# Performance work log

Measured on AMD Instinct MI355X. Metric: run time of the kernel, lower is better.

The kernel has to match this reference:

```python
import jax, jax.numpy as jnp
import numpy as np

N_STATES = 35
EMIT_SCALE = -500.0


def _constants():
    prior = jnp.full((N_STATES,), -10.0, dtype=jnp.float32).at[0].set(10.0)
    eye = jnp.eye(N_STATES, dtype=jnp.float32)
    trans = (0.1 * eye
             + 0.8 * jnp.roll(eye, 1, axis=1)
             + 0.08 * jnp.roll(eye, 2, axis=1)
             + (0.02 / N_STATES) * jnp.ones((N_STATES, N_STATES), dtype=jnp.float32))
    # Categorical(probs=trans).logits == log of row-normalized probs
    log_trans = jnp.log(trans / trans.sum(axis=-1, keepdims=True))
    return prior, log_trans


def setup_inputs() -> dict:
    key = jax.random.key(0)
    k1, k2 = jax.random.split(key)
    observations = jax.random.normal(k1, (64, 512, 16, 13, 12), dtype=jnp.float32)
    obs_matrix = jax.random.uniform(k2, (35, 16, 13, 12), dtype=jnp.float32)
    return {"observations": observations, "obs_matrix": obs_matrix}


def reference(observations, obs_matrix):
    prior, log_trans = _constants()
    B, T = observations.shape[:2]
    D = 16 * 13 * 12  # flattened frame dim = 2496
    x = observations.reshape(B, T, D)           # [B,T,D]
    m = obs_matrix.reshape(N_STATES, D)         # [S,D]
    x_sq = jnp.sum(x * x, axis=-1)              # [B,T]
    m_sq = jnp.sum(m * m, axis=-1)              # [S]
    xm = jnp.einsum('btd,sd->bts', x, m)        # [B,T,S]
    emis = (x_sq[..., None] + m_sq[None, None, :] - 2.0 * xm) / EMIT_SCALE  # [B,T,S]

    alpha0 = emis[:, 0] + prior                 # [B,S]
    log_trans_T = log_trans.T                   # [j,i] -> logT[i,j]

    def step(alpha, e_t):
        # alpha'[b,j] = e_t[b,j] + LSE_i(logT[i,j] + alpha[b,i])
        new = e_t + jax.nn.logsumexp(log_trans_T[None, :, :] + alpha[:, None, :], axis=2)
        return new, None

    emis_rest = jnp.swapaxes(emis[:, 1:], 0, 1)  # [T-1,B,S]
    alpha, _ = jax.lax.scan(step, alpha0, emis_rest)
    return jax.nn.logsumexp(alpha, axis=1)       # [B]
```

## Files before the change

### kernel.cpp

```cpp
#include <hip/hip_runtime.h>


#define ROWS 32768
#define KD   2496
#define NS   35
#define SPAD 48
#define ES   40
#define TT   512

typedef short v8s __attribute__((ext_vector_type(8)));
typedef float v4f __attribute__((ext_vector_type(4)));

__device__ __forceinline__ unsigned short f2bf(float f) {
    unsigned u = __builtin_bit_cast(unsigned, f);
    u += 0x7fffu + ((u >> 16) & 1u);
    return (unsigned short)(u >> 16);
}

template <int CTRL, int RM>
__device__ __forceinline__ float dppf(float oldv, float v) {
    return __builtin_bit_cast(float, __builtin_amdgcn_update_dpp(
        __builtin_bit_cast(int, oldv), __builtin_bit_cast(int, v),
        CTRL, RM, 0xf, false));
}

__device__ __forceinline__ float wsum63(float v) {
    v += dppf<0x111, 0xf>(0.f, v);
    v += dppf<0x112, 0xf>(0.f, v);
    v += dppf<0x114, 0xf>(0.f, v);
    v += dppf<0x118, 0xf>(0.f, v);
    v += dppf<0x142, 0xa>(0.f, v);
    v += dppf<0x143, 0xc>(0.f, v);
    return __builtin_bit_cast(float,
        __builtin_amdgcn_readlane(__builtin_bit_cast(int, v), 63));
}

__device__ __forceinline__ float wmax63(float v) {
    const float NI = -3.0e38f;
    v = fmaxf(v, dppf<0x111, 0xf>(NI, v));
    v = fmaxf(v, dppf<0x112, 0xf>(NI, v));
    v = fmaxf(v, dppf<0x114, 0xf>(NI, v));
    v = fmaxf(v, dppf<0x118, 0xf>(NI, v));
    v = fmaxf(v, dppf<0x142, 0xa>(NI, v));
    v = fmaxf(v, dppf<0x143, 0xc>(NI, v));
    return __builtin_bit_cast(float,
        __builtin_amdgcn_readlane(__builtin_bit_cast(int, v), 63));
}

__global__ __launch_bounds__(256) void prep_kernel(
        const float* __restrict__ m, unsigned short* __restrict__ mb,
        float* __restrict__ msq) {
    int s = blockIdx.x;
    int tid = threadIdx.x;
    float part = 0.f;
    for (int k = tid; k < KD; k += 256) {
        float v = (s < NS) ? m[s * KD + k] : 0.f;
        mb[s * KD + k] = f2bf(v);
        part += v * v;
    }
    __shared__ float red[256];
    red[tid] = part;
    __syncthreads();
    for (int off = 128; off > 0; off >>= 1) {
        if (tid < off) red[tid] += red[tid + off];
        __syncthreads();
    }
    if (tid == 0) msq[s] = red[0];
}

__global__ __launch_bounds__(256) void emis_kernel(
        const float* __restrict__ x, const unsigned short* __restrict__ mb,
        const float* __restrict__ msq, float* __restrict__ emis) {
    __shared__ short ldsA[64 * 104];
    __shared__ float sqpart[256];
    __shared__ float xsq[64];

    const int tid = threadIdx.x;
    const int row0 = blockIdx.x * 64;
    const int r = tid >> 2, c = tid & 3;
    const int lane = tid & 63, w = tid >> 6;
    const int fm = lane & 15, q = lane >> 4;
    const float* xr = x + (long)(row0 + r) * KD;

    float4 va[6];
#pragma unroll
    for (int i = 0; i < 6; ++i) va[i] = *(const float4*)&xr[4 * c + 16 * i];

    v4f acc[3] = {};
    float sq = 0.f;

    for (int kc = 0; kc < 26; ++kc) {
        const int k0 = kc * 96;
        v8s breg[3][3];
#pragma unroll
        for (int ks = 0; ks < 3; ++ks)
#pragma unroll
            for (int nt = 0; nt < 3; ++nt)
                breg[ks][nt] = *(const v8s*)&mb[(nt * 16 + fm) * KD + k0 + ks * 32 + q * 8];
#pragma unroll
        for (int i = 0; i < 6; ++i) {
            const float4 v = va[i];
            sq += v.x * v.x + v.y * v.y + v.z * v.z + v.w * v.w;
            unsigned lo = (unsigned)f2bf(v.x) | ((unsigned)f2bf(v.y) << 16);
            unsigned hi = (unsigned)f2bf(v.z) | ((unsigned)f2bf(v.w) << 16);
            *(uint2*)&ldsA[r * 104 + 4 * c + 16 * i] = make_uint2(lo, hi);
        }
        __syncthreads();
        if (kc + 1 < 26) {
            const float* xn = xr + (kc + 1) * 96;
#pragma unroll
            for (int i = 0; i < 6; ++i) va[i] = *(const float4*)&xn[4 * c + 16 * i];
        }
#pragma unroll
        for (int ks = 0; ks < 3; ++ks) {
            v8s a = *(const v8s*)&ldsA[(w * 16 + fm) * 104 + ks * 32 + q * 8];
#pragma unroll
            for (int nt = 0; nt < 3; ++nt)
                acc[nt] = __builtin_amdgcn_mfma_f32_16x16x32_bf16(a, breg[ks][nt], acc[nt], 0, 0, 0);
        }
        __syncthreads();
    }

    sqpart[tid] = sq;
    __syncthreads();
    if (tid < 64)
        xsq[tid] = sqpart[tid * 4] + sqpart[tid * 4 + 1] +
                   sqpart[tid * 4 + 2] + sqpart[tid * 4 + 3];
    __syncthreads();

#pragma unroll
    for (int nt = 0; nt < 3; ++nt) {
        const int st = nt * 16 + fm;
        if (st < NS) {
            const float ms = msq[st];
#pragma unroll
            for (int rg = 0; rg < 4; ++rg) {
                const int rl = w * 16 + q * 4 + rg;
                emis[(long)(row0 + rl) * ES + st] =
                    (xsq[rl] + ms - 2.f * acc[nt][rg]) * (-1.f / 500.f);
            }
        }
    }
}

__global__ __launch_bounds__(64) void forward_kernel(
        const float* __restrict__ emis, float* __restrict__ out) {
    const int b = blockIdx.x;
    const int j = threadIdx.x;
    const bool act = j < NS;
    const float LOG2E = 1.4426950408889634f, LN2 = 0.6931471805599453f;
    const float c0 = 0.1f, c1 = 0.8f, c2 = 0.08f, cb = 0.02f / 35.f;
    const float NI = -3.0e38f;

    const float* eb = emis + (long)b * TT * ES;
    const int s1 = (j + 34) % 35, s2 = (j + 33) % 35;

    const float e0 = act ? eb[j] : NI;
    const float a0 = e0 + ((j == 0) ? 10.f : -10.f);
    float C = wmax63(act ? a0 : NI);
    float p = act ? __builtin_amdgcn_exp2f((a0 - C) * LOG2E) : 0.f;

    float e_nx = eb[ES + j];
    for (int t = 1; t < TT; ++t) {
        const float ecur = e_nx;
        const int tn = (t + 1 < TT) ? (t + 1) : t;
        e_nx = eb[tn * ES + j];
        const float mx = wmax63(act ? ecur : NI);
        const float E = __builtin_amdgcn_exp2f((ecur - mx) * LOG2E);
        const float pm1 = __shfl(p, s1, 64);
        const float pm2 = __shfl(p, s2, 64);
        const float S = wsum63(p);
        float s = fmaf(c0, p, cb * S);
        s = fmaf(c1, pm1, s);
        s = fmaf(c2, pm2, s);
        p = act ? (E * s) : 0.f;
        C += mx;
        if ((t & 7) == 0) {
            p *= 1.0f / S;
            C += LN2 * __builtin_amdgcn_logf(S);
        }
    }
    const float Sf = wsum63(p);
    if (j == 0) out[b] = C + LN2 * __builtin_amdgcn_logf(Sf);
}

extern "C" void kernel_launch(void* const* d_in, const int* in_sizes, int n_in,
                              void* d_out, int out_size, void* d_ws, size_t ws_size,
                              hipStream_t stream) {
    const float* obs  = (const float*)d_in[0];
    const float* obsm = (const float*)d_in[1];
    float* out = (float*)d_out;

    char* ws = (char*)d_ws;
    float* emis = (float*)ws;
    unsigned short* mb = (unsigned short*)(ws + 5242880);
    float* msq = (float*)(ws + 5482496);

    prep_kernel<<<SPAD, 256, 0, stream>>>(obsm, mb, msq);
    emis_kernel<<<ROWS / 64, 256, 0, stream>>>(obs, mb, msq, emis);
    forward_kernel<<<64, 64, 0, stream>>>(emis, out);
}
```

Baseline: 562.4 us.

## Load MFMA operands directly to registers and batch-prefetch emissions in forward scan

The emission GEMM kernel drops the LDS staging and both block barriers. Each lane now loads its own A fragment from global memory, converts it to bf16 in registers, and double-buffers both A and B fragments across k-steps. Row sums of squares are reduced with cross-lane shuffles instead of shared memory. The forward scan prefetches eight timesteps of emissions at once, restructures the arithmetic slightly and hoists the renormalisation out of the inner loop. The cost is more register pressure and less coalesced 32-byte-per-lane strided global loads, in exchange for removing the barriers and LDS round-trips.

```diff
diff --git a/kernel.cpp b/kernel.cpp
--- a/kernel.cpp
+++ b/kernel.cpp
@@ -71,62 +71,72 @@
 __global__ __launch_bounds__(256) void emis_kernel(
         const float* __restrict__ x, const unsigned short* __restrict__ mb,
         const float* __restrict__ msq, float* __restrict__ emis) {
-    __shared__ short ldsA[64 * 104];
-    __shared__ float sqpart[256];
-    __shared__ float xsq[64];
-
     const int tid = threadIdx.x;
-    const int row0 = blockIdx.x * 64;
-    const int r = tid >> 2, c = tid & 3;
     const int lane = tid & 63, w = tid >> 6;
     const int fm = lane & 15, q = lane >> 4;
-    const float* xr = x + (long)(row0 + r) * KD;
-
-    float4 va[6];
-#pragma unroll
-    for (int i = 0; i < 6; ++i) va[i] = *(const float4*)&xr[4 * c + 16 * i];
+    const int row0 = blockIdx.x * 64 + w * 16;
+    const float* xr = x + (long)(row0 + fm) * KD + q * 8;
+    const unsigned short* mb0 = mb + (long)fm * KD + q * 8;
 
     v4f acc[3] = {};
     float sq = 0.f;
 
-    for (int kc = 0; kc < 26; ++kc) {
-        const int k0 = kc * 96;
-        v8s breg[3][3];
-#pragma unroll
-        for (int ks = 0; ks < 3; ++ks)
+    float4 cur[6][2], nxt[6][2];
+#pragma unroll
+    for (int i = 0; i < 6; ++i) {
+        cur[i][0] = *(const float4*)&xr[i * 32];
+        cur[i][1] = *(const float4*)&xr[i * 32 + 4];
+    }
+    v8s bc[3], bn[3];
+#pragma unroll
+    for (int nt = 0; nt < 3; ++nt)
+        bc[nt] = *(const v8s*)&mb0[nt * 16 * KD];
+
+    for (int g = 0; g < 13; ++g) {
+        const int kbase = g * 192;
+        if (g + 1 < 13) {
+            const float* xn = xr + kbase + 192;
+#pragma unroll
+            for (int i = 0; i < 6; ++i) {
+                nxt[i][0] = *(const float4*)&xn[i * 32];
+                nxt[i][1] = *(const float4*)&xn[i * 32 + 4];
+            }
+        }
+#pragma unroll
+        for (int i = 0; i < 6; ++i) {
+            const int knext = kbase + (i + 1) * 32;
+            if (knext < KD) {
+#pragma unroll
+                for (int nt = 0; nt < 3; ++nt)
+                    bn[nt] = *(const v8s*)&mb0[nt * 16 * KD + knext];
+            }
+            const float4 v0 = cur[i][0], v1 = cur[i][1];
+            sq += v0.x * v0.x + v0.y * v0.y + v0.z * v0.z + v0.w * v0.w
+                + v1.x * v1.x + v1.y * v1.y + v1.z * v1.z + v1.w * v1.w;
+            v8s a;
+            a[0] = (short)f2bf(v0.x); a[1] = (short)f2bf(v0.y);
+            a[2] = (short)f2bf(v0.z); a[3] = (short)f2bf(v0.w);
+            a[4] = (short)f2bf(v1.x); a[5] = (short)f2bf(v1.y);
+            a[6] = (short)f2bf(v1.z); a[7] = (short)f2bf(v1.w);
 #pragma unroll
             for (int nt = 0; nt < 3; ++nt)
-                breg[ks][nt] = *(const v8s*)&mb[(nt * 16 + fm) * KD + k0 + ks * 32 + q * 8];
+                acc[nt] = __builtin_amdgcn_mfma_f32_16x16x32_bf16(a, bc[nt], acc[nt], 0, 0, 0);
+#pragma unroll
+            for (int nt = 0; nt < 3; ++nt) bc[nt] = bn[nt];
+        }
 #pragma unroll
         for (int i = 0; i < 6; ++i) {
-            const float4 v = va[i];
-            sq += v.x * v.x + v.y * v.y + v.z * v.z + v.w * v.w;
-            unsigned lo = (unsigned)f2bf(v.x) | ((unsigned)f2bf(v.y) << 16);
-            unsigned hi = (unsigned)f2bf(v.z) | ((unsigned)f2bf(v.w) << 16);
-            *(uint2*)&ldsA[r * 104 + 4 * c + 16 * i] = make_uint2(lo, hi);
-        }
-        __syncthreads();
-        if (kc + 1 < 26) {
-            const float* xn = xr + (kc + 1) * 96;
-#pragma unroll
-            for (int i = 0; i < 6; ++i) va[i] = *(const float4*)&xn[4 * c + 16 * i];
-        }
-#pragma unroll
-        for (int ks = 0; ks < 3; ++ks) {
-            v8s a = *(const v8s*)&ldsA[(w * 16 + fm) * 104 + ks * 32 + q * 8];
-#pragma unroll
-            for (int nt = 0; nt < 3; ++nt)
-                acc[nt] = __builtin_amdgcn_mfma_f32_16x16x32_bf16(a, breg[ks][nt], acc[nt], 0, 0, 0);
-        }
-        __syncthreads();
-    }
-
-    sqpart[tid] = sq;
-    __syncthreads();
-    if (tid < 64)
-        xsq[tid] = sqpart[tid * 4] + sqpart[tid * 4 + 1] +
-                   sqpart[tid * 4 + 2] + sqpart[tid * 4 + 3];
-    __syncthreads();
+            cur[i][0] = nxt[i][0];
+            cur[i][1] = nxt[i][1];
+        }
+    }
+
+    float s2 = sq + __shfl_xor(sq, 16, 64);
+    s2 += __shfl_xor(s2, 32, 64);
+    float xs[4];
+#pragma unroll
+    for (int rg = 0; rg < 4; ++rg)
+        xs[rg] = __shfl(s2, q * 4 + rg, 64);
 
 #pragma unroll
     for (int nt = 0; nt < 3; ++nt) {
@@ -135,9 +145,8 @@
             const float ms = msq[st];
 #pragma unroll
             for (int rg = 0; rg < 4; ++rg) {
-                const int rl = w * 16 + q * 4 + rg;
-                emis[(long)(row0 + rl) * ES + st] =
-                    (xsq[rl] + ms - 2.f * acc[nt][rg]) * (-1.f / 500.f);
+                emis[(long)(row0 + q * 4 + rg) * ES + st] =
+                    (xs[rg] + ms - 2.f * acc[nt][rg]) * (-1.f / 500.f);
             }
         }
     }
@@ -148,37 +157,61 @@
     const int b = blockIdx.x;
     const int j = threadIdx.x;
     const bool act = j < NS;
+    const int jc = act ? j : NS - 1;
     const float LOG2E = 1.4426950408889634f, LN2 = 0.6931471805599453f;
     const float c0 = 0.1f, c1 = 0.8f, c2 = 0.08f, cb = 0.02f / 35.f;
     const float NI = -3.0e38f;
 
-    const float* eb = emis + (long)b * TT * ES;
+    const float* ebj = emis + (long)b * TT * ES + jc;
     const int s1 = (j + 34) % 35, s2 = (j + 33) % 35;
 
-    const float e0 = act ? eb[j] : NI;
-    const float a0 = e0 + ((j == 0) ? 10.f : -10.f);
+    const float e0 = ebj[0];
+    const float a0 = (act ? e0 : NI) + ((j == 0) ? 10.f : -10.f);
     float C = wmax63(act ? a0 : NI);
     float p = act ? __builtin_amdgcn_exp2f((a0 - C) * LOG2E) : 0.f;
 
-    float e_nx = eb[ES + j];
-    for (int t = 1; t < TT; ++t) {
-        const float ecur = e_nx;
-        const int tn = (t + 1 < TT) ? (t + 1) : t;
-        e_nx = eb[tn * ES + j];
-        const float mx = wmax63(act ? ecur : NI);
-        const float E = __builtin_amdgcn_exp2f((ecur - mx) * LOG2E);
+    float cur[8], nxt[8];
+#pragma unroll
+    for (int i = 0; i < 8; ++i) cur[i] = ebj[(1 + i) * ES];
+
+    for (int g = 0; g < 63; ++g) {
+        const int tb = 9 + 8 * g;
+#pragma unroll
+        for (int i = 0; i < 8; ++i) {
+            const int t = tb + i;
+            nxt[i] = ebj[(t < TT ? t : TT - 1) * ES];
+        }
+        float S = 1.f;
+#pragma unroll
+        for (int i = 0; i < 8; ++i) {
+            const float e = cur[i];
+            const float mx = wmax63(act ? e : NI);
+            const float E = act ? __builtin_amdgcn_exp2f((e - mx) * LOG2E) : 0.f;
+            const float pm1 = __shfl(p, s1, 64);
+            const float pm2 = __shfl(p, s2, 64);
+            S = wsum63(p);
+            const float u = fmaf(c1, pm1, c2 * pm2);
+            const float v = fmaf(c0, p, cb * S);
+            p = E * (u + v);
+            C += mx;
+        }
+        p *= 1.f / S;
+        C += LN2 * __builtin_amdgcn_logf(S);
+#pragma unroll
+        for (int i = 0; i < 8; ++i) cur[i] = nxt[i];
+    }
+#pragma unroll
+    for (int i = 0; i < 7; ++i) {
+        const float e = cur[i];
+        const float mx = wmax63(act ? e : NI);
+        const float E = act ? __builtin_amdgcn_exp2f((e - mx) * LOG2E) : 0.f;
         const float pm1 = __shfl(p, s1, 64);
         const float pm2 = __shfl(p, s2, 64);
         const float S = wsum63(p);
-        float s = fmaf(c0, p, cb * S);
-        s = fmaf(c1, pm1, s);
-        s = fmaf(c2, pm2, s);
-        p = act ? (E * s) : 0.f;
+        const float u = fmaf(c1, pm1, c2 * pm2);
+        const float v = fmaf(c0, p, cb * S);
+        p = E * (u + v);
         C += mx;
-        if ((t & 7) == 0) {
-            p *= 1.0f / S;
-            C += LN2 * __builtin_amdgcn_logf(S);
-        }
     }
     const float Sf = wsum63(p);
     if (j == 0) out[b] = C + LN2 * __builtin_amdgcn_logf(Sf);
```

Measured after the change: 523.6 us. -6.9%, faster.
